# Performance work log

Measured on AMD Instinct MI355X. Metric: run time of the kernel, lower is better.

Reference implementation:

```python
import jax, jax.numpy as jnp
import numpy as np
import math

BS, C, H, W, D = 2, 64, 32, 16, 32
FLAT = H * W * D          # 16384 voxels
N = 2048                  # non-empty voxels per sample (fixed for jit)
K = 256                   # min(int(0.2 * N), max_k=256)
EPS = 1e-5


def _pe(c, length):
    # sinusoidal positional encoding, interleaved sin/cos as in the torch code
    pos = jnp.arange(length, dtype=jnp.float32)[:, None]
    div = jnp.exp(jnp.arange(0, c, 2, dtype=jnp.float32) * (-math.log(10000.0) / c))
    ang = pos * div[None, :]                     # [length, c//2]
    return jnp.stack([jnp.sin(ang), jnp.cos(ang)], axis=-1).reshape(length, c)


def _bn(z, g, b):
    # eval-mode BatchNorm1d with running_mean=0, running_var=1
    return z * (g / jnp.sqrt(1.0 + EPS)) + b


def setup_inputs() -> dict:
    key = jax.random.key(0)
    ks = jax.random.split(key, 8)
    rng = np.random.default_rng(0)
    mask_idx = np.stack([np.sort(rng.choice(FLAT, size=N, replace=False)) for _ in range(BS)])
    w = lambda k, s: jax.random.normal(k, s, jnp.float32) * 0.05
    return dict(
        input=jax.random.normal(ks[0], (BS, C, H, W, D), jnp.float32),
        mask_idx=jnp.asarray(mask_idx, jnp.int32),
        w_ne1=w(ks[1], (C, 32)), b_ne1=jnp.zeros(32), g_ne=jnp.ones(32), be_ne=jnp.zeros(32),
        w_ne2=w(ks[2], (32, 1)), b_ne2=jnp.zeros(1),
        w_p1=w(ks[3], (C, 32)), b_p1=jnp.zeros(32), g_p1=jnp.ones(32), be_p1=jnp.zeros(32),
        w_p2=w(ks[4], (32, 32)), b_p2=jnp.zeros(32), g_p2=jnp.ones(32), be_p2=jnp.zeros(32),
        w_p3=w(ks[5], (32, 1)), b_p3=jnp.zeros(1),
        w_r1=w(ks[6], (4 * C, 2 * C)), b_r1=jnp.zeros(2 * C),
        w_r2=w(ks[7], (2 * C, C)), b_r2=jnp.zeros(C),
    )


def reference(input, mask_idx, w_ne1, b_ne1, g_ne, be_ne, w_ne2, b_ne2,
              w_p1, b_p1, g_p1, be_p1, w_p2, b_p2, g_p2, be_p2, w_p3, b_p3,
              w_r1, b_r1, w_r2, b_r2):
    bs, c = input.shape[0], input.shape[1]
    pe = _pe(c, FLAT)
    x = input                         # agg (external Bottleneck3D stack) ~ identity
    x_flat = x.reshape(bs, c, FLAT)

    def per_sample(xf, idx, key):
        mpe = pe[idx]                                  # [N, c] masked positional enc
        xi = xf[:, idx].T + mpe                        # [N, c] masked gather
        h1 = jax.nn.relu(_bn(xi @ w_ne1 + b_ne1, g_ne, be_ne))
        prob = jax.nn.sigmoid((h1 @ w_ne2 + b_ne2)[:, 0])    # [N] non-empty prob
        # torch.multinomial(prob, K, replacement=True)
        topk = jax.random.categorical(key, jnp.log(prob), shape=(K,))
        tf = xi[topk]                                  # [K, c] sampled features
        ne_k = prob[topk]                              # [K]
        # xi_repeat + tiled masked_pe[topk]  ->  [N, K, c]
        xw = xi[:, None, :] + mpe[topk][None, :, :]
        hp = jax.nn.relu(_bn(xw @ w_p1 + b_p1, g_p1, be_p1))
        hp = jax.nn.relu(_bn(hp @ w_p2 + b_p2, g_p2, be_p2))
        P = jax.nn.sigmoid((hp @ w_p3 + b_p3)[..., 0])  # [N, K]
        Pi = P * ne_k[None, :]
        Pe_ = (1.0 - P) * ne_k[None, :]
        x_intra = (Pi @ tf) / jnp.sum(Pi, axis=1, keepdims=True)   # [N, c]
        x_inter = (Pe_ @ tf) / jnp.sum(Pe_, axis=1, keepdims=True)
        ctx = jnp.zeros((2 * c, FLAT), input.dtype)
        ctx = ctx.at[:c, idx].set(x_intra.T).at[c:, idx].set(x_inter.T)
        return ctx

    keys = jax.random.split(jax.random.key(42), bs)
    ctx = jax.vmap(per_sample)(x_flat, mask_idx, keys).reshape(bs, 2 * c, H, W, D)
    xcat = jnp.concatenate([input, ctx, x], axis=1)     # [bs, 4c, H, W, D]
    # resize: the two defined 1x1 Conv3d layers (Bottleneck3D blocks are external)
    y = jnp.einsum('bchwd,cf->bfhwd', xcat, w_r1) + b_r1[None, :, None, None, None]
    y = jnp.einsum('bchwd,cf->bfhwd', y, w_r2) + b_r2[None, :, None, None, None]
    return y
```

## Files before the change

kernel.cpp:

```cpp
#include <hip/hip_runtime.h>
#include <cstdint>
#include <cmath>

#define BS    2
#define CC    64
#define FLAT  16384
#define NN    2048
#define KK    256
#define EPSBN 1e-5f
#define TINYF 1.17549435e-38f
#define PE_SCALE -0.14391156831212787f
#define JAX_PARTITIONABLE 1

#define OFF_XI    0
#define OFF_XI1   (OFF_XI   + BS*NN*CC)
#define OFF_PROB  (OFF_XI1  + BS*NN*32)
#define OFF_LOGP  (OFF_PROB + BS*NN)
#define OFF_NEK   (OFF_LOGP + BS*NN)
#define OFF_TF    (OFF_NEK  + BS*KK)
#define OFF_M1    (OFF_TF   + BS*KK*CC)
#define OFF_DELTA (OFF_M1   + BS*KK*32)
#define OFF_WF    (OFF_DELTA+ BS*NN*CC)
#define OFF_BF    (OFF_WF   + 256*CC)
#define OFF_INV   (OFF_BF   + CC)
#define OFF_PP    (OFF_INV  + BS*FLAT)

__device__ __forceinline__ uint32_t rotl32(uint32_t x, int r) {
  return (x << r) | (x >> (32 - r));
}
__device__ __forceinline__ void tf2x32(uint32_t k0, uint32_t k1,
                                       uint32_t& x0, uint32_t& x1) {
  uint32_t k2 = k0 ^ k1 ^ 0x1BD11BDAu;
  x0 += k0; x1 += k1;
#define TFR(r) { x0 += x1; x1 = rotl32(x1, r); x1 ^= x0; }
  TFR(13) TFR(15) TFR(26) TFR(6)  x0 += k1; x1 += k2 + 1u;
  TFR(17) TFR(29) TFR(16) TFR(24) x0 += k2; x1 += k0 + 2u;
  TFR(13) TFR(15) TFR(26) TFR(6)  x0 += k0; x1 += k1 + 3u;
  TFR(17) TFR(29) TFR(16) TFR(24) x0 += k1; x1 += k2 + 4u;
  TFR(13) TFR(15) TFR(26) TFR(6)  x0 += k2; x1 += k0 + 5u;
#undef TFR
}
__device__ __forceinline__ void jax_key(int b, uint32_t& k0, uint32_t& k1) {
#if JAX_PARTITIONABLE
  uint32_t x0 = 0u, x1 = (uint32_t)b;
  tf2x32(0u, 42u, x0, x1);
  k0 = x0; k1 = x1;
#else
  uint32_t a0 = 0u, a1 = 2u, c0 = 1u, c1 = 3u;
  tf2x32(0u, 42u, a0, a1);
  tf2x32(0u, 42u, c0, c1);
  if (b == 0) { k0 = a0; k1 = c0; } else { k0 = a1; k1 = c1; }
#endif
}
__device__ __forceinline__ uint32_t jax_bits(uint32_t k0, uint32_t k1, uint32_t i) {
#if JAX_PARTITIONABLE
  uint32_t x0 = 0u, x1 = i;
  tf2x32(k0, k1, x0, x1);
  return x0 ^ x1;
#else
  const uint32_t half = (uint32_t)(KK * NN) / 2u;
  uint32_t x0, x1;
  if (i < half) { x0 = i; x1 = i + half; tf2x32(k0, k1, x0, x1); return x0; }
  else          { x0 = i - half; x1 = i; tf2x32(k0, k1, x0, x1); return x1; }
#endif
}

__global__ void k0_fold(const float* __restrict__ w_r1, const float* __restrict__ b_r1,
                        const float* __restrict__ w_r2, const float* __restrict__ b_r2,
                        float* __restrict__ ws) {
  int c = blockIdx.x;
  int co = threadIdx.x;
  float acc = 0.f;
  for (int f = 0; f < 128; ++f)
    acc += w_r1[c * 128 + f] * w_r2[f * 64 + co];
  ws[OFF_WF + c * 64 + co] = acc;
  if (blockIdx.x == 0) {
    float bb = b_r2[co];
    for (int f = 0; f < 128; ++f) bb += b_r1[f] * w_r2[f * 64 + co];
    ws[OFF_BF + co] = bb;
  }
  int* inv = (int*)(ws + OFF_INV);
  int t = blockIdx.x * 64 + threadIdx.x;
  inv[t] = -1;
  inv[t + BS * FLAT / 2] = -1;
}

__global__ __launch_bounds__(256) void k1_xi(
    const float* __restrict__ input, const int* __restrict__ midx,
    const float* __restrict__ w_ne1, const float* __restrict__ b_ne1,
    const float* __restrict__ g_ne,  const float* __restrict__ be_ne,
    const float* __restrict__ w_ne2, const float* __restrict__ b_ne2,
    const float* __restrict__ w_p1,  const float* __restrict__ g_p1,
    float* __restrict__ ws) {
  int tid = threadIdx.x;
  int j = tid & 31, nl = tid >> 5;
  int bn = blockIdx.x * 8 + nl;
  int b = bn >> 11, n = bn & (NN - 1);
  int pos = midx[b * NN + n];
  __shared__ float xis[8][66];
  float d = expf((float)(2 * j) * PE_SCALE);
  float ang = (float)pos * d;
  float xs = sinf(ang) + input[((size_t)(b * CC + 2 * j)) * FLAT + pos];
  float xc = cosf(ang) + input[((size_t)(b * CC + 2 * j + 1)) * FLAT + pos];
  xis[nl][2 * j] = xs; xis[nl][2 * j + 1] = xc;
  float2 v2; v2.x = xs; v2.y = xc;
  ((float2*)(ws + OFF_XI + (size_t)(b * NN + n) * CC))[j] = v2;
  __syncthreads();
  float zne = b_ne1[j];
  float z1 = 0.f;
#pragma unroll
  for (int c2 = 0; c2 < CC; ++c2) {
    float xv = xis[nl][c2];
    zne += xv * w_ne1[c2 * 32 + j];
    z1  += xv * w_p1[c2 * 32 + j];
  }
  float ane = g_ne[j] / sqrtf(1.f + EPSBN);
  float h = fmaxf(0.f, zne * ane + be_ne[j]);
  float pp = h * w_ne2[j];
  for (int off = 16; off > 0; off >>= 1) pp += __shfl_down(pp, off, 32);
  if (j == 0) {
    float prob = 1.f / (1.f + expf(-(pp + b_ne2[0])));
    ws[OFF_PROB + b * NN + n] = prob;
    ws[OFF_LOGP + b * NN + n] = logf(prob);
    ((int*)(ws + OFF_INV))[b * FLAT + pos] = n;
  }
  float a1 = g_p1[j] / sqrtf(1.f + EPSBN);
  ws[OFF_XI1 + (size_t)(b * NN + n) * 32 + j] = z1 * a1;
}

__global__ __launch_bounds__(256) void k2_sample(
    const int* __restrict__ midx,
    const float* __restrict__ w_p1, const float* __restrict__ b_p1,
    const float* __restrict__ g_p1, const float* __restrict__ be_p1,
    float* __restrict__ ws) {
  int b = blockIdx.x >> 8, k = blockIdx.x & 255;
  int tid = threadIdx.x;
  uint32_t kb0, kb1;
  jax_key(b, kb0, kb1);
  const float* logp = ws + OFF_LOGP + b * NN;
  const float NEGINF = -__builtin_inff();
  float bv = NEGINF; int bn = NN;
#pragma unroll 1
  for (int r = 0; r < 8; ++r) {
    int n = r * 256 + tid;
    uint32_t bits = jax_bits(kb0, kb1, (uint32_t)(k * NN + n));
    float f = __uint_as_float(0x3f800000u | (bits >> 9)) - 1.0f;
    float u = fmaxf(TINYF, f + TINYF);
    float gmb = -logf(-logf(u));
    float v = logp[n] + gmb;
    if (v > bv || (v == bv && n < bn)) { bv = v; bn = n; }
  }
  __shared__ float sv[256];
  __shared__ int   sn[256];
  __shared__ float mpe[CC];
  sv[tid] = bv; sn[tid] = bn;
  __syncthreads();
  for (int s = 128; s > 0; s >>= 1) {
    if (tid < s) {
      float v2 = sv[tid + s]; int n2 = sn[tid + s];
      if (v2 > sv[tid] || (v2 == sv[tid] && n2 < sn[tid])) { sv[tid] = v2; sn[tid] = n2; }
    }
    __syncthreads();
  }
  int best = sn[0];
  if (tid == 0)
    ws[OFF_NEK + b * KK + k] = ws[OFF_PROB + b * NN + best];
  if (tid < CC) {
    int c = tid;
    ws[OFF_TF + (size_t)(b * KK + k) * CC + c] =
        ws[OFF_XI + (size_t)(b * NN + best) * CC + c];
    int pos = midx[b * NN + best];
    int jj = c >> 1;
    float ang = (float)pos * expf((float)(2 * jj) * PE_SCALE);
    mpe[c] = (c & 1) ? cosf(ang) : sinf(ang);
  }
  __syncthreads();
  if (tid < 32) {
    int jj = tid;
    float acc = b_p1[jj];
#pragma unroll
    for (int c = 0; c < CC; ++c) acc += mpe[c] * w_p1[c * 32 + jj];
    float a = g_p1[jj] / sqrtf(1.f + EPSBN);
    ws[OFF_M1 + (size_t)(b * KK + k) * 32 + jj] = acc * a + be_p1[jj];
  }
}

__global__ __launch_bounds__(256) void k3a_pairP(
    const float* __restrict__ w_p2, const float* __restrict__ b_p2,
    const float* __restrict__ g_p2, const float* __restrict__ be_p2,
    const float* __restrict__ w_p3, const float* __restrict__ b_p3,
    float* __restrict__ ws) {
  __shared__ __align__(16) float w2s[1024];
  __shared__ __align__(16) float hbuf[32 * 264];
  __shared__ __align__(16) float xi1s[4][32];
  __shared__ __align__(16) float c2f[32];
  __shared__ __align__(16) float w3l[32];
  int tid = threadIdx.x;
  int b = blockIdx.x >> 9;
  int n0 = (blockIdx.x & 511) * 4;
  int kg = tid >> 3, qg = tid & 7;
  int k0 = kg * 8, q0 = qg * 4;
  float m1r[32];
  {
    const float4* m4 = (const float4*)(ws + OFF_M1 + (size_t)(b * KK + tid) * 32);
#pragma unroll
    for (int q = 0; q < 8; ++q) {
      float4 v = m4[q];
      m1r[q * 4 + 0] = v.x; m1r[q * 4 + 1] = v.y;
      m1r[q * 4 + 2] = v.z; m1r[q * 4 + 3] = v.w;
    }
  }
  for (int e = tid; e < 1024; e += 256) {
    int jj = e & 31;
    w2s[e] = w_p2[e] * (g_p2[jj] / sqrtf(1.f + EPSBN));
  }
  if (tid < 32) {
    c2f[tid] = b_p2[tid] * (g_p2[tid] / sqrtf(1.f + EPSBN)) + be_p2[tid];
    w3l[tid] = w_p3[tid];
  }
  if (tid < 128) {
    int nn = tid >> 5, jx = tid & 31;
    xi1s[nn][jx] = ws[OFF_XI1 + (size_t)(b * NN + n0 + nn) * 32 + jx];
  }
  float nekv = ws[OFF_NEK + b * KK + tid];
  float b3 = b_p3[0];
  __syncthreads();
  const float4* w2s4 = (const float4*)w2s;
  const float4 cv = *(const float4*)&c2f[q0];
  const float4 w3v = *(const float4*)&w3l[q0];
#pragma unroll 1
  for (int nn = 0; nn < 4; ++nn) {
#pragma unroll
    for (int j = 0; j < 32; ++j)
      hbuf[j * 264 + tid] = fmaxf(0.f, xi1s[nn][j] + m1r[j]);
    __syncthreads();
    float z[8][4];
#pragma unroll
    for (int i = 0; i < 8; ++i) {
      z[i][0] = cv.x; z[i][1] = cv.y; z[i][2] = cv.z; z[i][3] = cv.w;
    }
#pragma unroll 8
    for (int jj = 0; jj < 32; ++jj) {
      float4 w = w2s4[jj * 8 + qg];
      const float4* mr = (const float4*)&hbuf[jj * 264 + k0];
      float4 ha = mr[0], hb = mr[1];
      z[0][0] += ha.x * w.x; z[0][1] += ha.x * w.y; z[0][2] += ha.x * w.z; z[0][3] += ha.x * w.w;
      z[1][0] += ha.y * w.x; z[1][1] += ha.y * w.y; z[1][2] += ha.y * w.z; z[1][3] += ha.y * w.w;
      z[2][0] += ha.z * w.x; z[2][1] += ha.z * w.y; z[2][2] += ha.z * w.z; z[2][3] += ha.z * w.w;
      z[3][0] += ha.w * w.x; z[3][1] += ha.w * w.y; z[3][2] += ha.w * w.z; z[3][3] += ha.w * w.w;
      z[4][0] += hb.x * w.x; z[4][1] += hb.x * w.y; z[4][2] += hb.x * w.z; z[4][3] += hb.x * w.w;
      z[5][0] += hb.y * w.x; z[5][1] += hb.y * w.y; z[5][2] += hb.y * w.z; z[5][3] += hb.y * w.w;
      z[6][0] += hb.z * w.x; z[6][1] += hb.z * w.y; z[6][2] += hb.z * w.z; z[6][3] += hb.z * w.w;
      z[7][0] += hb.w * w.x; z[7][1] += hb.w * w.y; z[7][2] += hb.w * w.z; z[7][3] += hb.w * w.w;
    }
    float s[8];
#pragma unroll
    for (int i = 0; i < 8; ++i)
      s[i] = fmaxf(0.f, z[i][0]) * w3v.x + fmaxf(0.f, z[i][1]) * w3v.y
           + fmaxf(0.f, z[i][2]) * w3v.z + fmaxf(0.f, z[i][3]) * w3v.w;
#pragma unroll
    for (int i = 0; i < 8; ++i) {
      s[i] += __shfl_xor(s[i], 1, 64);
      s[i] += __shfl_xor(s[i], 2, 64);
      s[i] += __shfl_xor(s[i], 4, 64);
    }
    float sv = qg < 4 ? (qg < 2 ? (qg == 0 ? s[0] : s[1]) : (qg == 2 ? s[2] : s[3]))
                      : (qg < 6 ? (qg == 4 ? s[4] : s[5]) : (qg == 6 ? s[6] : s[7]));
    float P = 1.f / (1.f + expf(-(sv + b3)));
    ws[OFF_PP + (size_t)(b * NN + n0 + nn) * KK + tid] = P * nekv;
    __syncthreads();
  }
}

__global__ __launch_bounds__(256) void k3b_ctx(
    float* __restrict__ ws) {
  __shared__ __align__(16) float Pis[4][256];
  __shared__ __align__(16) float nekl[256];
  __shared__ __align__(16) float xIl[4 * 68], xEl[4 * 68];
  __shared__ float sI[4], sE[4];
  int tid = threadIdx.x;
  int b = blockIdx.x >> 9;
  int n0 = (blockIdx.x & 511) * 4;
#pragma unroll
  for (int e = 0; e < 4; ++e)
    Pis[e][tid] = ws[OFF_PP + (size_t)(b * NN + n0 + e) * KK + tid];
  nekl[tid] = ws[OFF_NEK + b * KK + tid];
  __syncthreads();
  if (tid < 128) {
    int nn = tid >> 5, jx = tid & 31;
    float s1 = 0.f, s2 = 0.f;
#pragma unroll
    for (int t = 0; t < 8; ++t) {
      float pi = Pis[nn][jx + 32 * t];
      s1 += pi;
      s2 += nekl[jx + 32 * t] - pi;
    }
    for (int off = 16; off > 0; off >>= 1) {
      s1 += __shfl_down(s1, off, 32);
      s2 += __shfl_down(s2, off, 32);
    }
    if (jx == 0) { sI[nn] = s1; sE[nn] = s2; }
  }
  __syncthreads();
  {
    int c = tid & 63, n = tid >> 6;
    const float4* PI4 = (const float4*)Pis[n];
    const float4* NE4 = (const float4*)nekl;
    const float* tfg = ws + OFF_TF + (size_t)b * KK * CC + c;
    float aI = 0.f, aE = 0.f;
#pragma unroll 4
    for (int kq = 0; kq < 64; ++kq) {
      float4 piv = PI4[kq], nev = NE4[kq];
      float t0 = tfg[(4 * kq + 0) * 64];
      float t1 = tfg[(4 * kq + 1) * 64];
      float t2 = tfg[(4 * kq + 2) * 64];
      float t3 = tfg[(4 * kq + 3) * 64];
      aI += piv.x * t0 + piv.y * t1 + piv.z * t2 + piv.w * t3;
      aE += (nev.x - piv.x) * t0 + (nev.y - piv.y) * t1
          + (nev.z - piv.z) * t2 + (nev.w - piv.w) * t3;
    }
    xIl[n * 68 + c] = aI / sI[n];
    xEl[n * 68 + c] = aE / sE[n];
  }
  __syncthreads();
  {
    int co = tid & 63, nn = tid >> 6;
    const float4* xI4 = (const float4*)&xIl[nn * 68];
    const float4* xE4 = (const float4*)&xEl[nn * 68];
    const float* wI = ws + OFF_WF + 64 * CC + co;
    const float* wE = ws + OFF_WF + 128 * CC + co;
    float dsum = 0.f;
#pragma unroll 4
    for (int cq = 0; cq < 16; ++cq) {
      float4 xi4 = xI4[cq], xe4 = xE4[cq];
      dsum += xi4.x * wI[(4 * cq + 0) * 64] + xi4.y * wI[(4 * cq + 1) * 64]
            + xi4.z * wI[(4 * cq + 2) * 64] + xi4.w * wI[(4 * cq + 3) * 64];
      dsum += xe4.x * wE[(4 * cq + 0) * 64] + xe4.y * wE[(4 * cq + 1) * 64]
            + xe4.z * wE[(4 * cq + 2) * 64] + xe4.w * wE[(4 * cq + 3) * 64];
    }
    ws[OFF_DELTA + (size_t)(b * NN + n0 + nn) * CC + co] = dsum;
  }
}

__global__ __launch_bounds__(256) void k4_out(
    const float* __restrict__ input, float* __restrict__ out,
    const float* __restrict__ ws) {
  __shared__ __align__(16) float wfa[64 * 64];
  __shared__ float bfl[64];
  int tid = threadIdx.x;
  const float* wf = ws + OFF_WF;
  for (int e = tid; e < 4096; e += 256) {
    int c = e >> 6, co = e & 63;
    wfa[e] = wf[c * 64 + co] + wf[(192 + c) * 64 + co];
  }
  if (tid < 64) bfl[tid] = ws[OFF_BF + tid];
  __syncthreads();
  int q = tid >> 6, lane = tid & 63;
  int pg = blockIdx.x * 64 + lane;
  int b = pg >> 14, pos = pg & (FLAT - 1);
  const int* inv = (const int*)(ws + OFF_INV);
  float acc[16];
#pragma unroll
  for (int u = 0; u < 16; ++u) acc[u] = bfl[q * 16 + u];
#pragma unroll 4
  for (int c = 0; c < 64; ++c) {
    float xv = input[((size_t)(b * CC + c)) * FLAT + pos];
    const float4* wr = (const float4*)&wfa[c * 64 + q * 16];
#pragma unroll
    for (int u4 = 0; u4 < 4; ++u4) {
      float4 w = wr[u4];
      acc[u4 * 4 + 0] += xv * w.x; acc[u4 * 4 + 1] += xv * w.y;
      acc[u4 * 4 + 2] += xv * w.z; acc[u4 * 4 + 3] += xv * w.w;
    }
  }
  int n = inv[pg];
  if (n >= 0) {
    const float4* dr = (const float4*)(ws + OFF_DELTA + (size_t)(b * NN + n) * CC + q * 16);
#pragma unroll
    for (int u4 = 0; u4 < 4; ++u4) {
      float4 dv = dr[u4];
      acc[u4 * 4 + 0] += dv.x; acc[u4 * 4 + 1] += dv.y;
      acc[u4 * 4 + 2] += dv.z; acc[u4 * 4 + 3] += dv.w;
    }
  }
#pragma unroll
  for (int u = 0; u < 16; ++u)
    out[((size_t)(b * CC + q * 16 + u)) * FLAT + pos] = acc[u];
}

extern "C" void kernel_launch(void* const* d_in, const int* in_sizes, int n_in,
                              void* d_out, int out_size, void* d_ws, size_t ws_size,
                              hipStream_t stream) {
  const float* input = (const float*)d_in[0];
  const int*   midx  = (const int*)  d_in[1];
  const float* w_ne1 = (const float*)d_in[2];
  const float* b_ne1 = (const float*)d_in[3];
  const float* g_ne  = (const float*)d_in[4];
  const float* be_ne = (const float*)d_in[5];
  const float* w_ne2 = (const float*)d_in[6];
  const float* b_ne2 = (const float*)d_in[7];
  const float* w_p1  = (const float*)d_in[8];
  const float* b_p1  = (const float*)d_in[9];
  const float* g_p1  = (const float*)d_in[10];
  const float* be_p1 = (const float*)d_in[11];
  const float* w_p2  = (const float*)d_in[12];
  const float* b_p2  = (const float*)d_in[13];
  const float* g_p2  = (const float*)d_in[14];
  const float* be_p2 = (const float*)d_in[15];
  const float* w_p3  = (const float*)d_in[16];
  const float* b_p3  = (const float*)d_in[17];
  const float* w_r1  = (const float*)d_in[18];
  const float* b_r1  = (const float*)d_in[19];
  const float* w_r2  = (const float*)d_in[20];
  const float* b_r2  = (const float*)d_in[21];
  float* out = (float*)d_out;
  float* ws  = (float*)d_ws;

  k0_fold<<<dim3(256), dim3(64), 0, stream>>>(w_r1, b_r1, w_r2, b_r2, ws);
  k1_xi<<<dim3(BS * NN / 8), dim3(256), 0, stream>>>(
      input, midx, w_ne1, b_ne1, g_ne, be_ne, w_ne2, b_ne2, w_p1, g_p1, ws);
  k2_sample<<<dim3(BS * KK), dim3(256), 0, stream>>>(
      midx, w_p1, b_p1, g_p1, be_p1, ws);
  k3a_pairP<<<dim3(BS * NN / 4), dim3(256), 0, stream>>>(
      w_p2, b_p2, g_p2, be_p2, w_p3, b_p3, ws);
  k3b_ctx<<<dim3(BS * NN / 4), dim3(256), 0, stream>>>(ws);
  k4_out<<<dim3(BS * FLAT / 64), dim3(256), 0, stream>>>(input, out, ws);
}
```

Before: 190.9 us.

## Fuse pairwise probability and context kernels, keep probabilities in shared memory

Merges the pairwise MLP probability kernel with the context aggregation kernel, so the N×K probability matrix stays in shared memory instead of going through global memory. The inner MLP loop is also reorganised: each thread now computes 8 k × 8 output features for one n, reading a transposed M1 tile from LDS and recomputing the ReLU inline, rather than staging h in a per-n buffer. This removes a kernel launch and a large global write and read. In exchange the fused kernel uses more registers (a z[8][8] accumulator) and processes K in two halves with extra syncs, which could lower occupancy.

```diff
diff --git a/kernel.cpp b/kernel.cpp
--- a/kernel.cpp
+++ b/kernel.cpp
@@ -23,7 +23,6 @@
 #define OFF_WF    (OFF_DELTA+ BS*NN*CC)
 #define OFF_BF    (OFF_WF   + 256*CC)
 #define OFF_INV   (OFF_BF   + CC)
-#define OFF_PP    (OFF_INV  + BS*FLAT)
 
 __device__ __forceinline__ uint32_t rotl32(uint32_t x, int r) {
   return (x << r) | (x >> (32 - r));
@@ -185,113 +184,110 @@
   }
 }
 
-__global__ __launch_bounds__(256) void k3a_pairP(
+__global__ __launch_bounds__(256) void k3_fused(
     const float* __restrict__ w_p2, const float* __restrict__ b_p2,
     const float* __restrict__ g_p2, const float* __restrict__ be_p2,
     const float* __restrict__ w_p3, const float* __restrict__ b_p3,
     float* __restrict__ ws) {
+  __shared__ __align__(16) float m1t[32 * 132];
   __shared__ __align__(16) float w2s[1024];
-  __shared__ __align__(16) float hbuf[32 * 264];
+  __shared__ __align__(16) float Pis[4][256];
+  __shared__ __align__(16) float nekl[256];
   __shared__ __align__(16) float xi1s[4][32];
   __shared__ __align__(16) float c2f[32];
   __shared__ __align__(16) float w3l[32];
-  int tid = threadIdx.x;
-  int b = blockIdx.x >> 9;
-  int n0 = (blockIdx.x & 511) * 4;
-  int kg = tid >> 3, qg = tid & 7;
-  int k0 = kg * 8, q0 = qg * 4;
-  float m1r[32];
-  {
-    const float4* m4 = (const float4*)(ws + OFF_M1 + (size_t)(b * KK + tid) * 32);
-#pragma unroll
-    for (int q = 0; q < 8; ++q) {
-      float4 v = m4[q];
-      m1r[q * 4 + 0] = v.x; m1r[q * 4 + 1] = v.y;
-      m1r[q * 4 + 2] = v.z; m1r[q * 4 + 3] = v.w;
-    }
-  }
-  for (int e = tid; e < 1024; e += 256) {
-    int jj = e & 31;
-    w2s[e] = w_p2[e] * (g_p2[jj] / sqrtf(1.f + EPSBN));
-  }
-  if (tid < 32) {
-    c2f[tid] = b_p2[tid] * (g_p2[tid] / sqrtf(1.f + EPSBN)) + be_p2[tid];
-    w3l[tid] = w_p3[tid];
-  }
-  if (tid < 128) {
-    int nn = tid >> 5, jx = tid & 31;
-    xi1s[nn][jx] = ws[OFF_XI1 + (size_t)(b * NN + n0 + nn) * 32 + jx];
-  }
-  float nekv = ws[OFF_NEK + b * KK + tid];
-  float b3 = b_p3[0];
-  __syncthreads();
-  const float4* w2s4 = (const float4*)w2s;
-  const float4 cv = *(const float4*)&c2f[q0];
-  const float4 w3v = *(const float4*)&w3l[q0];
-#pragma unroll 1
-  for (int nn = 0; nn < 4; ++nn) {
-#pragma unroll
-    for (int j = 0; j < 32; ++j)
-      hbuf[j * 264 + tid] = fmaxf(0.f, xi1s[nn][j] + m1r[j]);
-    __syncthreads();
-    float z[8][4];
-#pragma unroll
-    for (int i = 0; i < 8; ++i) {
-      z[i][0] = cv.x; z[i][1] = cv.y; z[i][2] = cv.z; z[i][3] = cv.w;
-    }
-#pragma unroll 8
-    for (int jj = 0; jj < 32; ++jj) {
-      float4 w = w2s4[jj * 8 + qg];
-      const float4* mr = (const float4*)&hbuf[jj * 264 + k0];
-      float4 ha = mr[0], hb = mr[1];
-      z[0][0] += ha.x * w.x; z[0][1] += ha.x * w.y; z[0][2] += ha.x * w.z; z[0][3] += ha.x * w.w;
-      z[1][0] += ha.y * w.x; z[1][1] += ha.y * w.y; z[1][2] += ha.y * w.z; z[1][3] += ha.y * w.w;
-      z[2][0] += ha.z * w.x; z[2][1] += ha.z * w.y; z[2][2] += ha.z * w.z; z[2][3] += ha.z * w.w;
-      z[3][0] += ha.w * w.x; z[3][1] += ha.w * w.y; z[3][2] += ha.w * w.z; z[3][3] += ha.w * w.w;
-      z[4][0] += hb.x * w.x; z[4][1] += hb.x * w.y; z[4][2] += hb.x * w.z; z[4][3] += hb.x * w.w;
-      z[5][0] += hb.y * w.x; z[5][1] += hb.y * w.y; z[5][2] += hb.y * w.z; z[5][3] += hb.y * w.w;
-      z[6][0] += hb.z * w.x; z[6][1] += hb.z * w.y; z[6][2] += hb.z * w.z; z[6][3] += hb.z * w.w;
-      z[7][0] += hb.w * w.x; z[7][1] += hb.w * w.y; z[7][2] += hb.w * w.z; z[7][3] += hb.w * w.w;
-    }
-    float s[8];
-#pragma unroll
-    for (int i = 0; i < 8; ++i)
-      s[i] = fmaxf(0.f, z[i][0]) * w3v.x + fmaxf(0.f, z[i][1]) * w3v.y
-           + fmaxf(0.f, z[i][2]) * w3v.z + fmaxf(0.f, z[i][3]) * w3v.w;
-#pragma unroll
-    for (int i = 0; i < 8; ++i) {
-      s[i] += __shfl_xor(s[i], 1, 64);
-      s[i] += __shfl_xor(s[i], 2, 64);
-      s[i] += __shfl_xor(s[i], 4, 64);
-    }
-    float sv = qg < 4 ? (qg < 2 ? (qg == 0 ? s[0] : s[1]) : (qg == 2 ? s[2] : s[3]))
-                      : (qg < 6 ? (qg == 4 ? s[4] : s[5]) : (qg == 6 ? s[6] : s[7]));
-    float P = 1.f / (1.f + expf(-(sv + b3)));
-    ws[OFF_PP + (size_t)(b * NN + n0 + nn) * KK + tid] = P * nekv;
-    __syncthreads();
-  }
-}
-
-__global__ __launch_bounds__(256) void k3b_ctx(
-    float* __restrict__ ws) {
-  __shared__ __align__(16) float Pis[4][256];
-  __shared__ __align__(16) float nekl[256];
-  __shared__ __align__(16) float xIl[4 * 68], xEl[4 * 68];
   __shared__ float sI[4], sE[4];
   int tid = threadIdx.x;
   int b = blockIdx.x >> 9;
   int n0 = (blockIdx.x & 511) * 4;
-#pragma unroll
-  for (int e = 0; e < 4; ++e)
-    Pis[e][tid] = ws[OFF_PP + (size_t)(b * NN + n0 + e) * KK + tid];
+  int nn  = tid >> 6;
+  int kgl = (tid >> 2) & 15;
+  int qg  = tid & 3;
+  int k0l = kgl * 8, q0 = qg * 8;
+  for (int e = tid; e < 1024; e += 256) {
+    int q = e & 31;
+    w2s[e] = w_p2[e] * (g_p2[q] / sqrtf(1.f + EPSBN));
+  }
+  if (tid < 32) {
+    c2f[tid] = b_p2[tid] * (g_p2[tid] / sqrtf(1.f + EPSBN)) + be_p2[tid];
+    w3l[tid] = w_p3[tid];
+  }
+  if (tid < 128) {
+    int n4 = tid >> 5, jx = tid & 31;
+    xi1s[n4][jx] = ws[OFF_XI1 + (size_t)(b * NN + n0 + n4) * 32 + jx];
+  }
   nekl[tid] = ws[OFF_NEK + b * KK + tid];
-  __syncthreads();
+  float b3 = b_p3[0];
+  __syncthreads();
+  float4 cva = *(const float4*)&c2f[q0];
+  float4 cvb = *(const float4*)&c2f[q0 + 4];
+  float4 w3a = *(const float4*)&w3l[q0];
+  float4 w3b = *(const float4*)&w3l[q0 + 4];
+#pragma unroll 1
+  for (int kh = 0; kh < 2; ++kh) {
+    for (int e = tid; e < 1024; e += 256) {
+      int kl = e >> 3, q = e & 7;
+      float4 v = *(const float4*)(ws + OFF_M1 +
+                   (size_t)(b * KK + kh * 128 + kl) * 32 + q * 4);
+      m1t[(q * 4 + 0) * 132 + kl] = v.x;
+      m1t[(q * 4 + 1) * 132 + kl] = v.y;
+      m1t[(q * 4 + 2) * 132 + kl] = v.z;
+      m1t[(q * 4 + 3) * 132 + kl] = v.w;
+    }
+    __syncthreads();
+    float z[8][8];
+#pragma unroll
+    for (int i = 0; i < 8; ++i) {
+      z[i][0] = cva.x; z[i][1] = cva.y; z[i][2] = cva.z; z[i][3] = cva.w;
+      z[i][4] = cvb.x; z[i][5] = cvb.y; z[i][6] = cvb.z; z[i][7] = cvb.w;
+    }
+#pragma unroll 4
+    for (int jj = 0; jj < 32; ++jj) {
+      float xv = xi1s[nn][jj];
+      const float4* mr = (const float4*)&m1t[jj * 132 + k0l];
+      float4 ma = mr[0], mb = mr[1];
+      const float4* wr = (const float4*)&w2s[jj * 32 + q0];
+      float4 wa = wr[0], wb = wr[1];
+      float h0 = fmaxf(0.f, xv + ma.x), h1 = fmaxf(0.f, xv + ma.y);
+      float h2 = fmaxf(0.f, xv + ma.z), h3 = fmaxf(0.f, xv + ma.w);
+      float h4 = fmaxf(0.f, xv + mb.x), h5 = fmaxf(0.f, xv + mb.y);
+      float h6 = fmaxf(0.f, xv + mb.z), h7 = fmaxf(0.f, xv + mb.w);
+#define ZROW(i, hh) \
+      z[i][0] += hh * wa.x; z[i][1] += hh * wa.y; z[i][2] += hh * wa.z; z[i][3] += hh * wa.w; \
+      z[i][4] += hh * wb.x; z[i][5] += hh * wb.y; z[i][6] += hh * wb.z; z[i][7] += hh * wb.w;
+      ZROW(0, h0) ZROW(1, h1) ZROW(2, h2) ZROW(3, h3)
+      ZROW(4, h4) ZROW(5, h5) ZROW(6, h6) ZROW(7, h7)
+#undef ZROW
+    }
+    float s[8];
+#pragma unroll
+    for (int i = 0; i < 8; ++i)
+      s[i] = fmaxf(0.f, z[i][0]) * w3a.x + fmaxf(0.f, z[i][1]) * w3a.y
+           + fmaxf(0.f, z[i][2]) * w3a.z + fmaxf(0.f, z[i][3]) * w3a.w
+           + fmaxf(0.f, z[i][4]) * w3b.x + fmaxf(0.f, z[i][5]) * w3b.y
+           + fmaxf(0.f, z[i][6]) * w3b.z + fmaxf(0.f, z[i][7]) * w3b.w;
+#pragma unroll
+    for (int i = 0; i < 8; ++i) {
+      s[i] += __shfl_xor(s[i], 1, 64);
+      s[i] += __shfl_xor(s[i], 2, 64);
+    }
+    float sv0 = qg < 2 ? (qg == 0 ? s[0] : s[1]) : (qg == 2 ? s[2] : s[3]);
+    float sv1 = qg < 2 ? (qg == 0 ? s[4] : s[5]) : (qg == 2 ? s[6] : s[7]);
+    int kg0 = kh * 128 + k0l;
+    float P0 = 1.f / (1.f + expf(-(sv0 + b3)));
+    float P1 = 1.f / (1.f + expf(-(sv1 + b3)));
+    Pis[nn][kg0 + qg]     = P0 * nekl[kg0 + qg];
+    Pis[nn][kg0 + 4 + qg] = P1 * nekl[kg0 + 4 + qg];
+    __syncthreads();
+  }
+  float* xIl = m1t;
+  float* xEl = m1t + 272;
   if (tid < 128) {
-    int nn = tid >> 5, jx = tid & 31;
+    int n4 = tid >> 5, jx = tid & 31;
     float s1 = 0.f, s2 = 0.f;
 #pragma unroll
     for (int t = 0; t < 8; ++t) {
-      float pi = Pis[nn][jx + 32 * t];
+      float pi = Pis[n4][jx + 32 * t];
       s1 += pi;
       s2 += nekl[jx + 32 * t] - pi;
     }
@@ -299,7 +295,7 @@
       s1 += __shfl_down(s1, off, 32);
       s2 += __shfl_down(s2, off, 32);
     }
-    if (jx == 0) { sI[nn] = s1; sE[nn] = s2; }
+    if (jx == 0) { sI[n4] = s1; sE[n4] = s2; }
   }
   __syncthreads();
   {
@@ -324,9 +320,9 @@
   }
   __syncthreads();
   {
-    int co = tid & 63, nn = tid >> 6;
-    const float4* xI4 = (const float4*)&xIl[nn * 68];
-    const float4* xE4 = (const float4*)&xEl[nn * 68];
+    int co = tid & 63, n4 = tid >> 6;
+    const float4* xI4 = (const float4*)&xIl[n4 * 68];
+    const float4* xE4 = (const float4*)&xEl[n4 * 68];
     const float* wI = ws + OFF_WF + 64 * CC + co;
     const float* wE = ws + OFF_WF + 128 * CC + co;
     float dsum = 0.f;
@@ -338,7 +334,7 @@
       dsum += xe4.x * wE[(4 * cq + 0) * 64] + xe4.y * wE[(4 * cq + 1) * 64]
             + xe4.z * wE[(4 * cq + 2) * 64] + xe4.w * wE[(4 * cq + 3) * 64];
     }
-    ws[OFF_DELTA + (size_t)(b * NN + n0 + nn) * CC + co] = dsum;
+    ws[OFF_DELTA + (size_t)(b * NN + n0 + n4) * CC + co] = dsum;
   }
 }
 
@@ -421,8 +417,7 @@
       input, midx, w_ne1, b_ne1, g_ne, be_ne, w_ne2, b_ne2, w_p1, g_p1, ws);
   k2_sample<<<dim3(BS * KK), dim3(256), 0, stream>>>(
       midx, w_p1, b_p1, g_p1, be_p1, ws);
-  k3a_pairP<<<dim3(BS * NN / 4), dim3(256), 0, stream>>>(
+  k3_fused<<<dim3(BS * NN / 4), dim3(256), 0, stream>>>(
       w_p2, b_p2, g_p2, be_p2, w_p3, b_p3, ws);
-  k3b_ctx<<<dim3(BS * NN / 4), dim3(256), 0, stream>>>(ws);
   k4_out<<<dim3(BS * FLAT / 64), dim3(256), 0, stream>>>(input, out, ws);
 }
```

Result: faster. 182.1 us (-4.6%).
